# Performance work log

Hardware: AMD Instinct MI355X
Metric: run time of the kernel (lower is better)

The kernel has to match this reference:

```python
import jax, jax.numpy as jnp
import numpy as np

P = 16          # patch size
D = 256         # emb dim
NH = 4          # attention heads
DH = D // NH    # head dim
GS = 4          # LE-fusion group size
EPS = 1e-5
ALPHA = 1.0
DELTA = 1.0
BETA = 1.0


def setup_inputs() -> dict:
    key = jax.random.key(0)
    ks = jax.random.split(key, 12)
    B, C, H, W = 8, 1, 256, 256
    s = 0.02
    return {
        "x": jax.random.normal(ks[0], (B, C, H, W), jnp.float32),
        # patch embed as matmul over flattened patches (equivalent to Conv2d k=s=P)
        "Wp": jax.random.normal(ks[1], (C * P * P, D), jnp.float32) * s,
        "bp": jnp.zeros((D,), jnp.float32),
        "ln_g": jnp.ones((D,), jnp.float32),
        "ln_b": jnp.zeros((D,), jnp.float32),
        "Wq": jax.random.normal(ks[2], (D, D), jnp.float32) * s,
        "bq": jnp.zeros((D,), jnp.float32),
        "Wk": jax.random.normal(ks[3], (D, D), jnp.float32) * s,
        "bk": jnp.zeros((D,), jnp.float32),
        "Wv": jax.random.normal(ks[4], (D, D), jnp.float32) * s,
        "bv": jnp.zeros((D,), jnp.float32),
        "Wo": jax.random.normal(ks[5], (D, D), jnp.float32) * s,
        "bo": jnp.zeros((D,), jnp.float32),
    }


def _forward(x, Wp, bp, ln_g, ln_b, Wq, bq, Wk, bk, Wv, bv, Wo, bo):
    B, C, H, W = x.shape
    nh, nw = H // P, W // P
    N = nh * nw
    # --- patch embed: (B,C,H,W) -> (B,N,C*P*P) @ Wp ---
    patches = x.reshape(B, C, nh, P, nw, P).transpose(0, 2, 4, 1, 3, 5)
    patches = patches.reshape(B, N, C * P * P)
    z = patches @ Wp + bp  # (B, N, D)
    # --- NF-Norm: LayerNorm then NeuroFocal scaling ---
    mu = z.mean(-1, keepdims=True)
    var = ((z - mu) ** 2).mean(-1, keepdims=True)
    zn = (z - mu) * jax.lax.rsqrt(var + EPS) * ln_g + ln_b
    mu2 = zn.mean(-1, keepdims=True)
    var2 = ((zn - mu2) ** 2).mean(-1, keepdims=True)
    nf = jnp.abs(zn - mu2).sum(-1, keepdims=True) / (jnp.sqrt(var2 + EPS) + EPS)
    z = zn * (1.0 + nf)
    # --- AG-NFA attention ---
    def split(t):  # (B,N,D) -> (B,NH,N,DH)
        return t.reshape(B, N, NH, DH).transpose(0, 2, 1, 3)
    Q = split(z @ Wq + bq)
    K = split(z @ Wk + bk)
    V = split(z @ Wv + bv)
    qk = jnp.einsum("bhnd,bhmd->bhnm", Q, K)
    logits = qk / jnp.sqrt(jnp.float32(DH))
    mu_q = Q.mean(-1, keepdims=True)
    var_q = ((Q - mu_q) ** 2).mean(-1, keepdims=True)
    sigma_q = jnp.sqrt(var_q + EPS)
    nf_q = jnp.abs(Q - mu_q).sum(-1, keepdims=True) / (sigma_q + EPS)  # (B,NH,N,1)
    # ||Q_n - K_m||^2 = |Q|^2 + |K|^2 - 2 Q.K  (avoids O(N^2*d) diff tensor)
    q2 = (Q * Q).sum(-1)  # (B,NH,N)
    k2 = (K * K).sum(-1)  # (B,NH,N)
    omega = q2[..., :, None] + k2[..., None, :] - 2.0 * qk
    omega = omega / (jnp.exp(-DELTA * nf_q) + 1.0)
    A = jax.nn.softmax(logits - ALPHA * omega, axis=-1)
    out = jnp.einsum("bhnm,bhmd->bhnd", A, V)
    out = out.transpose(0, 2, 1, 3).reshape(B, N, D)
    Y = out @ Wo + bo
    # --- LE-Fusion ---
    G = N // GS
    Yg = Y.reshape(B, G, GS, D)
    E = jnp.linalg.norm(Yg, axis=-1)  # (B,G,GS)
    lam = jax.nn.softmax(BETA * E, axis=-1)[..., None]
    return (lam * Yg).sum(axis=2)  # (B, G, D)


def reference(x, Wp, bp, ln_g, ln_b, Wq, bq, Wk, bk, Wv, bv, Wo, bo):
    return _forward(x, Wp, bp, ln_g, ln_b, Wq, bq, Wk, bk, Wv, bv, Wo, bo)
```

## Files before the change

### kernel.cpp

```cpp
#include <hip/hip_runtime.h>

#define EPSF 1e-5f
#define KSTR 68
#define PSTR 260

#define FMA4(ACC, ZS, WV) \
    ACC.x = fmaf(ZS, WV.x, ACC.x); ACC.y = fmaf(ZS, WV.y, ACC.y); \
    ACC.z = fmaf(ZS, WV.z, ACC.z); ACC.w = fmaf(ZS, WV.w, ACC.w);

__global__ __launch_bounds__(512, 2) void ka_patch_nf_qkv(
    const float* __restrict__ x,
    const float* __restrict__ Wp, const float* __restrict__ bp,
    const float* __restrict__ ln_g, const float* __restrict__ ln_b,
    const float* __restrict__ Wq, const float* __restrict__ bq,
    const float* __restrict__ Wk, const float* __restrict__ bk,
    const float* __restrict__ Wv, const float* __restrict__ bv,
    float* __restrict__ Qg, float* __restrict__ Kg, float* __restrict__ Vg)
{
    extern __shared__ float sm[];
    float* zr = sm;
    float* ps = sm + 2048;

    const int tid = threadIdx.x;
    const int kq = tid >> 7, tg = (tid >> 6) & 1, ln = tid & 63;
    const int wave = tid >> 6, lane = tid & 63;
    const int tok0 = blockIdx.x * 8;
    const int tg4 = 4 * tg;

    #pragma unroll
    for (int i = 0; i < 4; ++i) {
        int e = tid + 512 * i;
        int t = e >> 8, dd = e & 255;
        int tk = tok0 + t, b = tk >> 8, n = tk & 255;
        int ph = n >> 4, pw = n & 15, p = dd >> 4, q = dd & 15;
        zr[t * 256 + dd] = x[b * 65536 + (ph * 16 + p) * 256 + pw * 16 + q];
    }
    __syncthreads();

    {
        const float* wr = Wp + kq * 16384 + 4 * ln;
        const float* zb = zr + tg4 * 256 + kq * 64;
        float4 a0 = make_float4(0.f,0.f,0.f,0.f), a1 = a0, a2 = a0, a3 = a0;
        #pragma unroll
        for (int kk = 0; kk < 64; kk += 8) {
            float4 w0 = *(const float4*)(wr + (kk + 0) * 256);
            float4 w1 = *(const float4*)(wr + (kk + 1) * 256);
            float4 w2 = *(const float4*)(wr + (kk + 2) * 256);
            float4 w3 = *(const float4*)(wr + (kk + 3) * 256);
            float4 w4 = *(const float4*)(wr + (kk + 4) * 256);
            float4 w5 = *(const float4*)(wr + (kk + 5) * 256);
            float4 w6 = *(const float4*)(wr + (kk + 6) * 256);
            float4 w7 = *(const float4*)(wr + (kk + 7) * 256);
            float4 zA0 = *(const float4*)(zb + 0 * 256 + kk);
            float4 zA1 = *(const float4*)(zb + 0 * 256 + kk + 4);
            float4 zB0 = *(const float4*)(zb + 1 * 256 + kk);
            float4 zB1 = *(const float4*)(zb + 1 * 256 + kk + 4);
            float4 zC0 = *(const float4*)(zb + 2 * 256 + kk);
            float4 zC1 = *(const float4*)(zb + 2 * 256 + kk + 4);
            float4 zD0 = *(const float4*)(zb + 3 * 256 + kk);
            float4 zD1 = *(const float4*)(zb + 3 * 256 + kk + 4);
            FMA4(a0, zA0.x, w0) FMA4(a0, zA0.y, w1) FMA4(a0, zA0.z, w2) FMA4(a0, zA0.w, w3)
            FMA4(a0, zA1.x, w4) FMA4(a0, zA1.y, w5) FMA4(a0, zA1.z, w6) FMA4(a0, zA1.w, w7)
            FMA4(a1, zB0.x, w0) FMA4(a1, zB0.y, w1) FMA4(a1, zB0.z, w2) FMA4(a1, zB0.w, w3)
            FMA4(a1, zB1.x, w4) FMA4(a1, zB1.y, w5) FMA4(a1, zB1.z, w6) FMA4(a1, zB1.w, w7)
            FMA4(a2, zC0.x, w0) FMA4(a2, zC0.y, w1) FMA4(a2, zC0.z, w2) FMA4(a2, zC0.w, w3)
            FMA4(a2, zC1.x, w4) FMA4(a2, zC1.y, w5) FMA4(a2, zC1.z, w6) FMA4(a2, zC1.w, w7)
            FMA4(a3, zD0.x, w0) FMA4(a3, zD0.y, w1) FMA4(a3, zD0.z, w2) FMA4(a3, zD0.w, w3)
            FMA4(a3, zD1.x, w4) FMA4(a3, zD1.y, w5) FMA4(a3, zD1.z, w6) FMA4(a3, zD1.w, w7)
        }
        float* pp = ps + kq * 2048 + tg4 * 256 + 4 * ln;
        *(float4*)(pp + 0 * 256) = a0;
        *(float4*)(pp + 1 * 256) = a1;
        *(float4*)(pp + 2 * 256) = a2;
        *(float4*)(pp + 3 * 256) = a3;
    }
    __syncthreads();
    {
        int e = tid * 4;
        float4 u0 = *(float4*)(ps + e);
        float4 u1 = *(float4*)(ps + 2048 + e);
        float4 u2 = *(float4*)(ps + 4096 + e);
        float4 u3 = *(float4*)(ps + 6144 + e);
        float4 bb = *(const float4*)(bp + (e & 255));
        float4 z;
        z.x = (u0.x + u1.x) + (u2.x + u3.x) + bb.x;
        z.y = (u0.y + u1.y) + (u2.y + u3.y) + bb.y;
        z.z = (u0.z + u1.z) + (u2.z + u3.z) + bb.z;
        z.w = (u0.w + u1.w) + (u2.w + u3.w) + bb.w;
        *(float4*)(zr + e) = z;
    }
    __syncthreads();

    {
        float g[4], bb2[4], v[4];
        #pragma unroll
        for (int c = 0; c < 4; ++c) { g[c] = ln_g[lane + 64 * c]; bb2[c] = ln_b[lane + 64 * c]; }
        float s = 0.f, ss = 0.f;
        #pragma unroll
        for (int c = 0; c < 4; ++c) { v[c] = zr[wave * 256 + lane + 64 * c]; s += v[c]; ss += v[c] * v[c]; }
        #pragma unroll
        for (int o = 32; o; o >>= 1) { s += __shfl_xor(s, o); ss += __shfl_xor(ss, o); }
        float mu  = s * (1.f / 256.f);
        float var = ss * (1.f / 256.f) - mu * mu;
        float rs  = rsqrtf(var + EPSF);
        float zn[4]; float s2 = 0.f, ss2 = 0.f;
        #pragma unroll
        for (int c = 0; c < 4; ++c) {
            zn[c] = (v[c] - mu) * rs * g[c] + bb2[c];
            s2 += zn[c]; ss2 += zn[c] * zn[c];
        }
        #pragma unroll
        for (int o = 32; o; o >>= 1) { s2 += __shfl_xor(s2, o); ss2 += __shfl_xor(ss2, o); }
        float mu2  = s2 * (1.f / 256.f);
        float var2 = ss2 * (1.f / 256.f) - mu2 * mu2;
        float as = 0.f;
        #pragma unroll
        for (int c = 0; c < 4; ++c) as += fabsf(zn[c] - mu2);
        #pragma unroll
        for (int o = 32; o; o >>= 1) as += __shfl_xor(as, o);
        float nf = as / (sqrtf(var2 + EPSF) + EPSF);
        float sc = 1.f + nf;
        #pragma unroll
        for (int c = 0; c < 4; ++c) zr[wave * 256 + lane + 64 * c] = zn[c] * sc;
    }
    __syncthreads();

    {
        const float* qr = Wq + kq * 16384 + 4 * ln;
        const float* kr = Wk + kq * 16384 + 4 * ln;
        const float* vr = Wv + kq * 16384 + 4 * ln;
        const float* zb = zr + tg4 * 256 + kq * 64;
        float4 aq0 = make_float4(0.f,0.f,0.f,0.f), aq1 = aq0, aq2 = aq0, aq3 = aq0;
        float4 ak0 = aq0, ak1 = aq0, ak2 = aq0, ak3 = aq0;
        float4 av0 = aq0, av1 = aq0, av2 = aq0, av3 = aq0;
        #pragma unroll
        for (int kk = 0; kk < 64; kk += 4) {
            float4 qw0 = *(const float4*)(qr + (kk + 0) * 256);
            float4 qw1 = *(const float4*)(qr + (kk + 1) * 256);
            float4 qw2 = *(const float4*)(qr + (kk + 2) * 256);
            float4 qw3 = *(const float4*)(qr + (kk + 3) * 256);
            float4 kw0 = *(const float4*)(kr + (kk + 0) * 256);
            float4 kw1 = *(const float4*)(kr + (kk + 1) * 256);
            float4 kw2 = *(const float4*)(kr + (kk + 2) * 256);
            float4 kw3 = *(const float4*)(kr + (kk + 3) * 256);
            float4 vw0 = *(const float4*)(vr + (kk + 0) * 256);
            float4 vw1 = *(const float4*)(vr + (kk + 1) * 256);
            float4 vw2 = *(const float4*)(vr + (kk + 2) * 256);
            float4 vw3 = *(const float4*)(vr + (kk + 3) * 256);
            float4 zA = *(const float4*)(zb + 0 * 256 + kk);
            float4 zB = *(const float4*)(zb + 1 * 256 + kk);
            float4 zC = *(const float4*)(zb + 2 * 256 + kk);
            float4 zD = *(const float4*)(zb + 3 * 256 + kk);
            FMA4(aq0, zA.x, qw0) FMA4(aq0, zA.y, qw1) FMA4(aq0, zA.z, qw2) FMA4(aq0, zA.w, qw3)
            FMA4(ak0, zA.x, kw0) FMA4(ak0, zA.y, kw1) FMA4(ak0, zA.z, kw2) FMA4(ak0, zA.w, kw3)
            FMA4(av0, zA.x, vw0) FMA4(av0, zA.y, vw1) FMA4(av0, zA.z, vw2) FMA4(av0, zA.w, vw3)
            FMA4(aq1, zB.x, qw0) FMA4(aq1, zB.y, qw1) FMA4(aq1, zB.z, qw2) FMA4(aq1, zB.w, qw3)
            FMA4(ak1, zB.x, kw0) FMA4(ak1, zB.y, kw1) FMA4(ak1, zB.z, kw2) FMA4(ak1, zB.w, kw3)
            FMA4(av1, zB.x, vw0) FMA4(av1, zB.y, vw1) FMA4(av1, zB.z, vw2) FMA4(av1, zB.w, vw3)
            FMA4(aq2, zC.x, qw0) FMA4(aq2, zC.y, qw1) FMA4(aq2, zC.z, qw2) FMA4(aq2, zC.w, qw3)
            FMA4(ak2, zC.x, kw0) FMA4(ak2, zC.y, kw1) FMA4(ak2, zC.z, kw2) FMA4(ak2, zC.w, kw3)
            FMA4(av2, zC.x, vw0) FMA4(av2, zC.y, vw1) FMA4(av2, zC.z, vw2) FMA4(av2, zC.w, vw3)
            FMA4(aq3, zD.x, qw0) FMA4(aq3, zD.y, qw1) FMA4(aq3, zD.z, qw2) FMA4(aq3, zD.w, qw3)
            FMA4(ak3, zD.x, kw0) FMA4(ak3, zD.y, kw1) FMA4(ak3, zD.z, kw2) FMA4(ak3, zD.w, kw3)
            FMA4(av3, zD.x, vw0) FMA4(av3, zD.y, vw1) FMA4(av3, zD.z, vw2) FMA4(av3, zD.w, vw3)
        }
        float* pq = ps + kq * 2048 + tg4 * 256 + 4 * ln;
        *(float4*)(pq + 0 * 256) = aq0;
        *(float4*)(pq + 1 * 256) = aq1;
        *(float4*)(pq + 2 * 256) = aq2;
        *(float4*)(pq + 3 * 256) = aq3;
        float* pk = pq + 8192;
        *(float4*)(pk + 0 * 256) = ak0;
        *(float4*)(pk + 1 * 256) = ak1;
        *(float4*)(pk + 2 * 256) = ak2;
        *(float4*)(pk + 3 * 256) = ak3;
        float* pv = pq + 16384;
        *(float4*)(pv + 0 * 256) = av0;
        *(float4*)(pv + 1 * 256) = av1;
        *(float4*)(pv + 2 * 256) = av2;
        *(float4*)(pv + 3 * 256) = av3;
    }
    __syncthreads();

    {
        int e = tid * 4, t = e >> 8, d0 = e & 255;
        int tk = tok0 + t, b = tk >> 8, n = tk & 255;
        int h = d0 >> 6, dh = d0 & 63;
        #pragma unroll
        for (int mat = 0; mat < 3; ++mat) {
            const float* pr = ps + mat * 8192;
            float4 u0 = *(float4*)(pr + e);
            float4 u1 = *(float4*)(pr + 2048 + e);
            float4 u2 = *(float4*)(pr + 4096 + e);
            float4 u3 = *(float4*)(pr + 6144 + e);
            const float* bsrc = (mat == 0) ? bq : (mat == 1) ? bk : bv;
            float4 bb = *(const float4*)(bsrc + d0);
            float4 o;
            o.x = (u0.x + u1.x) + (u2.x + u3.x) + bb.x;
            o.y = (u0.y + u1.y) + (u2.y + u3.y) + bb.y;
            o.z = (u0.z + u1.z) + (u2.z + u3.z) + bb.z;
            o.w = (u0.w + u1.w) + (u2.w + u3.w) + bb.w;
            float* gout = ((mat == 0) ? Qg : (mat == 1) ? Kg : Vg)
                        + ((b * 4 + h) * 256 + n) * 64 + dh;
            *(float4*)gout = o;
        }
    }
}

__global__ __launch_bounds__(512, 2) void kb_attn(
    const float* __restrict__ Qg, const float* __restrict__ Kg,
    const float* __restrict__ Vg, float* __restrict__ Og)
{
    extern __shared__ float lds[];
    float* Kl = lds;
    float* k2 = lds + 256 * KSTR;
    float* Pl = lds;

    const int tid = threadIdx.x;
    const int xcd = blockIdx.x & 7, slot = blockIdx.x >> 3;
    const int bh = xcd * 4 + (slot >> 3);
    const int qt = slot & 7;

    const float* Qb = Qg + (bh * 256 + qt * 32) * 64;
    const float* Kb = Kg + bh * 16384;
    const float* Vb = Vg + bh * 16384;

    const int q = tid >> 4;
    const int r = tid & 15;

    {
        const float4* Ks = (const float4*)Kb;
        #pragma unroll
        for (int i = 0; i < 8; ++i) {
            int flat = tid + 512 * i;
            int row = flat >> 4, c4 = flat & 15;
            *(float4*)(Kl + row * KSTR + c4 * 4) = Ks[flat];
        }
    }
    __syncthreads();

    {
        int row = tid >> 1, half = tid & 1;
        const float* kp = Kl + row * KSTR + half * 32;
        float ssq = 0.f;
        #pragma unroll
        for (int c = 0; c < 8; ++c) {
            float4 kv = *(const float4*)(kp + 4 * c);
            ssq += kv.x*kv.x + kv.y*kv.y + kv.z*kv.z + kv.w*kv.w;
        }
        ssq += __shfl_xor(ssq, 1);
        if (half == 0) k2[row] = ssq;
    }

    float4 Qr[16];
    {
        const float4* Qp = (const float4*)(Qb + q * 64);
        #pragma unroll
        for (int c = 0; c < 16; ++c) Qr[c] = Qp[c];
    }
    float fq, gq, iq;
    {
        float s = 0.f, ss = 0.f;
        #pragma unroll
        for (int c = 0; c < 16; ++c) {
            float4 v = Qr[c];
            s  += v.x + v.y + v.z + v.w;
            ss += v.x*v.x + v.y*v.y + v.z*v.z + v.w*v.w;
        }
        float mu = s * (1.f / 64.f);
        float as = 0.f;
        #pragma unroll
        for (int c = 0; c < 16; ++c) {
            float4 v = Qr[c];
            as += fabsf(v.x - mu) + fabsf(v.y - mu)
                + fabsf(v.z - mu) + fabsf(v.w - mu);
        }
        float var = ss * (1.f / 64.f) - mu * mu;
        float sg  = sqrtf(var + EPSF);
        float nf  = as / (sg + EPSF);
        float inv = 1.f / (__expf(-nf) + 1.f);
        fq = 0.125f + 2.f * inv;
        gq = ss * inv;
        iq = inv;
    }
    __syncthreads();

    float s_[16];
    #pragma unroll
    for (int j = 0; j < 16; ++j) {
        int m = r + 16 * j;
        const float* kp = Kl + m * KSTR;
        float acc = 0.f;
        #pragma unroll
        for (int c = 0; c < 16; ++c) {
            float4 kv = *(const float4*)(kp + 4 * c);
            acc += Qr[c].x*kv.x + Qr[c].y*kv.y + Qr[c].z*kv.z + Qr[c].w*kv.w;
        }
        s_[j] = acc * fq - gq - k2[m] * iq;
    }

    float M = s_[0];
    #pragma unroll
    for (int j = 1; j < 16; ++j) M = fmaxf(M, s_[j]);
    #pragma unroll
    for (int o = 1; o < 16; o <<= 1) M = fmaxf(M, __shfl_xor(M, o));
    float L = 0.f;
    #pragma unroll
    for (int j = 0; j < 16; ++j) { s_[j] = __expf(s_[j] - M); L += s_[j]; }
    #pragma unroll
    for (int o = 1; o < 16; o <<= 1) L += __shfl_xor(L, o);
    float invL = 1.f / L;

    __syncthreads();
    #pragma unroll
    for (int j = 0; j < 16; ++j) Pl[q * PSTR + r + 16 * j] = s_[j] * invL;
    __syncthreads();

    float4 a0 = make_float4(0.f, 0.f, 0.f, 0.f);
    const float* pq = Pl + q * PSTR;
    #pragma unroll 8
    for (int m = 0; m < 256; ++m) {
        float pw = pq[m];
        float4 v = *(const float4*)(Vb + m * 64 + 4 * r);
        a0.x = fmaf(pw, v.x, a0.x); a0.y = fmaf(pw, v.y, a0.y);
        a0.z = fmaf(pw, v.z, a0.z); a0.w = fmaf(pw, v.w, a0.w);
    }
    {
        int b = bh >> 2, h = bh & 3;
        int n = qt * 32 + q;
        float* op = Og + (b * 256 + n) * 256 + h * 64 + 4 * r;
        *(float4*)op = a0;
    }
}

__global__ __launch_bounds__(512, 2) void kc_wo_le(
    const float* __restrict__ Og, const float* __restrict__ Wo,
    const float* __restrict__ bo, float* __restrict__ out)
{
    __shared__ __align__(16) float sm[2048 + 8192 + 8];
    float* yr  = sm;
    float* ps  = sm + 2048;
    float* red = sm + 10240;

    const int tid = threadIdx.x;
    const int kq = tid >> 7, tg = (tid >> 6) & 1, ln = tid & 63;
    const int wave = tid >> 6, lane = tid & 63;
    const int tok0 = blockIdx.x * 8;
    const int tg4 = 4 * tg;

    *(float4*)(yr + tid * 4) = *(const float4*)(Og + tok0 * 256 + tid * 4);
    __syncthreads();

    {
        const float* wr = Wo + kq * 16384 + 4 * ln;
        const float* zb = yr + tg4 * 256 + kq * 64;
        float4 a0 = make_float4(0.f,0.f,0.f,0.f), a1 = a0, a2 = a0, a3 = a0;
        #pragma unroll
        for (int kk = 0; kk < 64; kk += 8) {
            float4 w0 = *(const float4*)(wr + (kk + 0) * 256);
            float4 w1 = *(const float4*)(wr + (kk + 1) * 256);
            float4 w2 = *(const float4*)(wr + (kk + 2) * 256);
            float4 w3 = *(const float4*)(wr + (kk + 3) * 256);
            float4 w4 = *(const float4*)(wr + (kk + 4) * 256);
            float4 w5 = *(const float4*)(wr + (kk + 5) * 256);
            float4 w6 = *(const float4*)(wr + (kk + 6) * 256);
            float4 w7 = *(const float4*)(wr + (kk + 7) * 256);
            float4 zA0 = *(const float4*)(zb + 0 * 256 + kk);
            float4 zA1 = *(const float4*)(zb + 0 * 256 + kk + 4);
            float4 zB0 = *(const float4*)(zb + 1 * 256 + kk);
            float4 zB1 = *(const float4*)(zb + 1 * 256 + kk + 4);
            float4 zC0 = *(const float4*)(zb + 2 * 256 + kk);
            float4 zC1 = *(const float4*)(zb + 2 * 256 + kk + 4);
            float4 zD0 = *(const float4*)(zb + 3 * 256 + kk);
            float4 zD1 = *(const float4*)(zb + 3 * 256 + kk + 4);
            FMA4(a0, zA0.x, w0) FMA4(a0, zA0.y, w1) FMA4(a0, zA0.z, w2) FMA4(a0, zA0.w, w3)
            FMA4(a0, zA1.x, w4) FMA4(a0, zA1.y, w5) FMA4(a0, zA1.z, w6) FMA4(a0, zA1.w, w7)
            FMA4(a1, zB0.x, w0) FMA4(a1, zB0.y, w1) FMA4(a1, zB0.z, w2) FMA4(a1, zB0.w, w3)
            FMA4(a1, zB1.x, w4) FMA4(a1, zB1.y, w5) FMA4(a1, zB1.z, w6) FMA4(a1, zB1.w, w7)
            FMA4(a2, zC0.x, w0) FMA4(a2, zC0.y, w1) FMA4(a2, zC0.z, w2) FMA4(a2, zC0.w, w3)
            FMA4(a2, zC1.x, w4) FMA4(a2, zC1.y, w5) FMA4(a2, zC1.z, w6) FMA4(a2, zC1.w, w7)
            FMA4(a3, zD0.x, w0) FMA4(a3, zD0.y, w1) FMA4(a3, zD0.z, w2) FMA4(a3, zD0.w, w3)
            FMA4(a3, zD1.x, w4) FMA4(a3, zD1.y, w5) FMA4(a3, zD1.z, w6) FMA4(a3, zD1.w, w7)
        }
        float* pp = ps + kq * 2048 + tg4 * 256 + 4 * ln;
        *(float4*)(pp + 0 * 256) = a0;
        *(float4*)(pp + 1 * 256) = a1;
        *(float4*)(pp + 2 * 256) = a2;
        *(float4*)(pp + 3 * 256) = a3;
    }
    __syncthreads();
    {
        int e = tid * 4;
        float4 u0 = *(float4*)(ps + e);
        float4 u1 = *(float4*)(ps + 2048 + e);
        float4 u2 = *(float4*)(ps + 4096 + e);
        float4 u3 = *(float4*)(ps + 6144 + e);
        float4 bb = *(const float4*)(bo + (e & 255));
        float4 y;
        y.x = (u0.x + u1.x) + (u2.x + u3.x) + bb.x;
        y.y = (u0.y + u1.y) + (u2.y + u3.y) + bb.y;
        y.z = (u0.z + u1.z) + (u2.z + u3.z) + bb.z;
        y.w = (u0.w + u1.w) + (u2.w + u3.w) + bb.w;
        *(float4*)(yr + e) = y;
    }
    __syncthreads();
    {
        float ssq = 0.f;
        #pragma unroll
        for (int c = 0; c < 4; ++c) {
            float v = yr[wave * 256 + lane + 64 * c];
            ssq += v * v;
        }
        #pragma unroll
        for (int o = 32; o; o >>= 1) ssq += __shfl_xor(ssq, o);
        if (lane == 0) red[wave] = sqrtf(ssq);
    }
    __syncthreads();
    {
        int g = tid >> 8, d = tid & 255;
        float e0 = red[4 * g], e1 = red[4 * g + 1], e2 = red[4 * g + 2], e3 = red[4 * g + 3];
        float m = fmaxf(fmaxf(e0, e1), fmaxf(e2, e3));
        float x0 = __expf(e0 - m), x1 = __expf(e1 - m), x2 = __expf(e2 - m), x3 = __expf(e3 - m);
        float inv = 1.f / (x0 + x1 + x2 + x3);
        float val = (x0 * yr[(4 * g) * 256 + d] + x1 * yr[(4 * g + 1) * 256 + d]
                   + x2 * yr[(4 * g + 2) * 256 + d] + x3 * yr[(4 * g + 3) * 256 + d]) * inv;
        out[(blockIdx.x * 2 + g) * 256 + d] = val;
    }
}

extern "C" void kernel_launch(void* const* d_in, const int* in_sizes, int n_in,
                              void* d_out, int out_size, void* d_ws, size_t ws_size,
                              hipStream_t stream) {
    const float* x    = (const float*)d_in[0];
    const float* Wp   = (const float*)d_in[1];
    const float* bp   = (const float*)d_in[2];
    const float* ln_g = (const float*)d_in[3];
    const float* ln_b = (const float*)d_in[4];
    const float* Wq   = (const float*)d_in[5];
    const float* bq   = (const float*)d_in[6];
    const float* Wk   = (const float*)d_in[7];
    const float* bk   = (const float*)d_in[8];
    const float* Wv   = (const float*)d_in[9];
    const float* bv   = (const float*)d_in[10];
    const float* Wo   = (const float*)d_in[11];
    const float* bo   = (const float*)d_in[12];
    float* out = (float*)d_out;

    float* ws = (float*)d_ws;
    const size_t TKD = 2048 * 64 * 4;
    float* Qg = ws;
    float* Kg = ws + TKD;
    float* Vg = ws + 2 * TKD;
    float* Og = ws + 3 * TKD;

    const int ka_lds = (2048 + 3 * 4 * 2048) * 4;
    const int kb_lds = (256 * KSTR + 256) * 4;
    (void)hipFuncSetAttribute((const void*)ka_patch_nf_qkv,
                              hipFuncAttributeMaxDynamicSharedMemorySize, ka_lds);
    (void)hipFuncSetAttribute((const void*)kb_attn,
                              hipFuncAttributeMaxDynamicSharedMemorySize, kb_lds);

    ka_patch_nf_qkv<<<256, 512, ka_lds, stream>>>(x, Wp, bp, ln_g, ln_b,
                                                  Wq, bq, Wk, bk, Wv, bv, Qg, Kg, Vg);
    kb_attn<<<256, 512, kb_lds, stream>>>(Qg, Kg, Vg, Og);
    kc_wo_le<<<256, 512, 0, stream>>>(Og, Wo, bo, out);
}
```

Baseline: 60.70 us.

## Fuse three kernels into one cooperative kernel with grid syncs

Merges the patch/NF/QKV, attention and Wo/LE-fusion kernels into a single cooperative launch of 256 blocks, with grid.sync() between the stages in place of kernel boundaries. The aim is to remove launch overhead and the gaps between the three dependent kernels. In exchange the whole grid must be co-resident, LDS sizing is set to the largest stage, and grid-wide barriers carry their own cost.

```diff
diff --git a/kernel.cpp b/kernel.cpp
--- a/kernel.cpp
+++ b/kernel.cpp
@@ -1,4 +1,7 @@
 #include <hip/hip_runtime.h>
+#include <hip/hip_cooperative_groups.h>
+
+namespace cg = cooperative_groups;
 
 #define EPSF 1e-5f
 #define KSTR 68
@@ -8,423 +11,425 @@
     ACC.x = fmaf(ZS, WV.x, ACC.x); ACC.y = fmaf(ZS, WV.y, ACC.y); \
     ACC.z = fmaf(ZS, WV.z, ACC.z); ACC.w = fmaf(ZS, WV.w, ACC.w);
 
-__global__ __launch_bounds__(512, 2) void ka_patch_nf_qkv(
+__global__ __launch_bounds__(512, 2) void mega(
     const float* __restrict__ x,
     const float* __restrict__ Wp, const float* __restrict__ bp,
     const float* __restrict__ ln_g, const float* __restrict__ ln_b,
     const float* __restrict__ Wq, const float* __restrict__ bq,
     const float* __restrict__ Wk, const float* __restrict__ bk,
     const float* __restrict__ Wv, const float* __restrict__ bv,
-    float* __restrict__ Qg, float* __restrict__ Kg, float* __restrict__ Vg)
+    const float* __restrict__ Wo, const float* __restrict__ bo,
+    float* __restrict__ Qg, float* __restrict__ Kg, float* __restrict__ Vg,
+    float* __restrict__ Og, float* __restrict__ out)
 {
     extern __shared__ float sm[];
-    float* zr = sm;
-    float* ps = sm + 2048;
+    cg::grid_group grid = cg::this_grid();
 
     const int tid = threadIdx.x;
-    const int kq = tid >> 7, tg = (tid >> 6) & 1, ln = tid & 63;
-    const int wave = tid >> 6, lane = tid & 63;
-    const int tok0 = blockIdx.x * 8;
-    const int tg4 = 4 * tg;
-
-    #pragma unroll
-    for (int i = 0; i < 4; ++i) {
-        int e = tid + 512 * i;
-        int t = e >> 8, dd = e & 255;
-        int tk = tok0 + t, b = tk >> 8, n = tk & 255;
-        int ph = n >> 4, pw = n & 15, p = dd >> 4, q = dd & 15;
-        zr[t * 256 + dd] = x[b * 65536 + (ph * 16 + p) * 256 + pw * 16 + q];
+    const int bid = blockIdx.x;
+
+    {
+        float* zr = sm;
+        float* ps = sm + 2048;
+
+        const int kq = tid >> 7, tg = (tid >> 6) & 1, ln = tid & 63;
+        const int wave = tid >> 6, lane = tid & 63;
+        const int tok0 = bid * 8;
+        const int tg4 = 4 * tg;
+
+        #pragma unroll
+        for (int i = 0; i < 4; ++i) {
+            int e = tid + 512 * i;
+            int t = e >> 8, dd = e & 255;
+            int tk = tok0 + t, b = tk >> 8, n = tk & 255;
+            int ph = n >> 4, pw = n & 15, p = dd >> 4, q = dd & 15;
+            zr[t * 256 + dd] = x[b * 65536 + (ph * 16 + p) * 256 + pw * 16 + q];
+        }
+        __syncthreads();
+
+        {
+            const float* wr = Wp + kq * 16384 + 4 * ln;
+            const float* zb = zr + tg4 * 256 + kq * 64;
+            float4 a0 = make_float4(0.f,0.f,0.f,0.f), a1 = a0, a2 = a0, a3 = a0;
+            #pragma unroll
+            for (int kk = 0; kk < 64; kk += 8) {
+                float4 w0 = *(const float4*)(wr + (kk + 0) * 256);
+                float4 w1 = *(const float4*)(wr + (kk + 1) * 256);
+                float4 w2 = *(const float4*)(wr + (kk + 2) * 256);
+                float4 w3 = *(const float4*)(wr + (kk + 3) * 256);
+                float4 w4 = *(const float4*)(wr + (kk + 4) * 256);
+                float4 w5 = *(const float4*)(wr + (kk + 5) * 256);
+                float4 w6 = *(const float4*)(wr + (kk + 6) * 256);
+                float4 w7 = *(const float4*)(wr + (kk + 7) * 256);
+                float4 zA0 = *(const float4*)(zb + 0 * 256 + kk);
+                float4 zA1 = *(const float4*)(zb + 0 * 256 + kk + 4);
+                float4 zB0 = *(const float4*)(zb + 1 * 256 + kk);
+                float4 zB1 = *(const float4*)(zb + 1 * 256 + kk + 4);
+                float4 zC0 = *(const float4*)(zb + 2 * 256 + kk);
+                float4 zC1 = *(const float4*)(zb + 2 * 256 + kk + 4);
+                float4 zD0 = *(const float4*)(zb + 3 * 256 + kk);
+                float4 zD1 = *(const float4*)(zb + 3 * 256 + kk + 4);
+                FMA4(a0, zA0.x, w0) FMA4(a0, zA0.y, w1) FMA4(a0, zA0.z, w2) FMA4(a0, zA0.w, w3)
+                FMA4(a0, zA1.x, w4) FMA4(a0, zA1.y, w5) FMA4(a0, zA1.z, w6) FMA4(a0, zA1.w, w7)
+                FMA4(a1, zB0.x, w0) FMA4(a1, zB0.y, w1) FMA4(a1, zB0.z, w2) FMA4(a1, zB0.w, w3)
+                FMA4(a1, zB1.x, w4) FMA4(a1, zB1.y, w5) FMA4(a1, zB1.z, w6) FMA4(a1, zB1.w, w7)
+                FMA4(a2, zC0.x, w0) FMA4(a2, zC0.y, w1) FMA4(a2, zC0.z, w2) FMA4(a2, zC0.w, w3)
+                FMA4(a2, zC1.x, w4) FMA4(a2, zC1.y, w5) FMA4(a2, zC1.z, w6) FMA4(a2, zC1.w, w7)
+                FMA4(a3, zD0.x, w0) FMA4(a3, zD0.y, w1) FMA4(a3, zD0.z, w2) FMA4(a3, zD0.w, w3)
+                FMA4(a3, zD1.x, w4) FMA4(a3, zD1.y, w5) FMA4(a3, zD1.z, w6) FMA4(a3, zD1.w, w7)
+            }
+            float* pp = ps + kq * 2048 + tg4 * 256 + 4 * ln;
+            *(float4*)(pp + 0 * 256) = a0;
+            *(float4*)(pp + 1 * 256) = a1;
+            *(float4*)(pp + 2 * 256) = a2;
+            *(float4*)(pp + 3 * 256) = a3;
+        }
+        __syncthreads();
+        {
+            int e = tid * 4;
+            float4 u0 = *(float4*)(ps + e);
+            float4 u1 = *(float4*)(ps + 2048 + e);
+            float4 u2 = *(float4*)(ps + 4096 + e);
+            float4 u3 = *(float4*)(ps + 6144 + e);
+            float4 bb = *(const float4*)(bp + (e & 255));
+            float4 z;
+            z.x = (u0.x + u1.x) + (u2.x + u3.x) + bb.x;
+            z.y = (u0.y + u1.y) + (u2.y + u3.y) + bb.y;
+            z.z = (u0.z + u1.z) + (u2.z + u3.z) + bb.z;
+            z.w = (u0.w + u1.w) + (u2.w + u3.w) + bb.w;
+            *(float4*)(zr + e) = z;
+        }
+        __syncthreads();
+
+        {
+            float g[4], bb2[4], v[4];
+            #pragma unroll
+            for (int c = 0; c < 4; ++c) { g[c] = ln_g[lane + 64 * c]; bb2[c] = ln_b[lane + 64 * c]; }
+            float s = 0.f, ss = 0.f;
+            #pragma unroll
+            for (int c = 0; c < 4; ++c) { v[c] = zr[wave * 256 + lane + 64 * c]; s += v[c]; ss += v[c] * v[c]; }
+            #pragma unroll
+            for (int o = 32; o; o >>= 1) { s += __shfl_xor(s, o); ss += __shfl_xor(ss, o); }
+            float mu  = s * (1.f / 256.f);
+            float var = ss * (1.f / 256.f) - mu * mu;
+            float rs  = rsqrtf(var + EPSF);
+            float zn[4]; float s2 = 0.f, ss2 = 0.f;
+            #pragma unroll
+            for (int c = 0; c < 4; ++c) {
+                zn[c] = (v[c] - mu) * rs * g[c] + bb2[c];
+                s2 += zn[c]; ss2 += zn[c] * zn[c];
+            }
+            #pragma unroll
+            for (int o = 32; o; o >>= 1) { s2 += __shfl_xor(s2, o); ss2 += __shfl_xor(ss2, o); }
+            float mu2  = s2 * (1.f / 256.f);
+            float var2 = ss2 * (1.f / 256.f) - mu2 * mu2;
+            float as = 0.f;
+            #pragma unroll
+            for (int c = 0; c < 4; ++c) as += fabsf(zn[c] - mu2);
+            #pragma unroll
+            for (int o = 32; o; o >>= 1) as += __shfl_xor(as, o);
+            float nf = as / (sqrtf(var2 + EPSF) + EPSF);
+            float sc = 1.f + nf;
+            #pragma unroll
+            for (int c = 0; c < 4; ++c) zr[wave * 256 + lane + 64 * c] = zn[c] * sc;
+        }
+        __syncthreads();
+
+        {
+            const float* qr = Wq + kq * 16384 + 4 * ln;
+            const float* kr = Wk + kq * 16384 + 4 * ln;
+            const float* vr = Wv + kq * 16384 + 4 * ln;
+            const float* zb = zr + tg4 * 256 + kq * 64;
+            float4 aq0 = make_float4(0.f,0.f,0.f,0.f), aq1 = aq0, aq2 = aq0, aq3 = aq0;
+            float4 ak0 = aq0, ak1 = aq0, ak2 = aq0, ak3 = aq0;
+            float4 av0 = aq0, av1 = aq0, av2 = aq0, av3 = aq0;
+            #pragma unroll
+            for (int kk = 0; kk < 64; kk += 4) {
+                float4 qw0 = *(const float4*)(qr + (kk + 0) * 256);
+                float4 qw1 = *(const float4*)(qr + (kk + 1) * 256);
+                float4 qw2 = *(const float4*)(qr + (kk + 2) * 256);
+                float4 qw3 = *(const float4*)(qr + (kk + 3) * 256);
+                float4 kw0 = *(const float4*)(kr + (kk + 0) * 256);
+                float4 kw1 = *(const float4*)(kr + (kk + 1) * 256);
+                float4 kw2 = *(const float4*)(kr + (kk + 2) * 256);
+                float4 kw3 = *(const float4*)(kr + (kk + 3) * 256);
+                float4 vw0 = *(const float4*)(vr + (kk + 0) * 256);
+                float4 vw1 = *(const float4*)(vr + (kk + 1) * 256);
+                float4 vw2 = *(const float4*)(vr + (kk + 2) * 256);
+                float4 vw3 = *(const float4*)(vr + (kk + 3) * 256);
+                float4 zA = *(const float4*)(zb + 0 * 256 + kk);
+                float4 zB = *(const float4*)(zb + 1 * 256 + kk);
+                float4 zC = *(const float4*)(zb + 2 * 256 + kk);
+                float4 zD = *(const float4*)(zb + 3 * 256 + kk);
+                FMA4(aq0, zA.x, qw0) FMA4(aq0, zA.y, qw1) FMA4(aq0, zA.z, qw2) FMA4(aq0, zA.w, qw3)
+                FMA4(ak0, zA.x, kw0) FMA4(ak0, zA.y, kw1) FMA4(ak0, zA.z, kw2) FMA4(ak0, zA.w, kw3)
+                FMA4(av0, zA.x, vw0) FMA4(av0, zA.y, vw1) FMA4(av0, zA.z, vw2) FMA4(av0, zA.w, vw3)
+                FMA4(aq1, zB.x, qw0) FMA4(aq1, zB.y, qw1) FMA4(aq1, zB.z, qw2) FMA4(aq1, zB.w, qw3)
+                FMA4(ak1, zB.x, kw0) FMA4(ak1, zB.y, kw1) FMA4(ak1, zB.z, kw2) FMA4(ak1, zB.w, kw3)
+                FMA4(av1, zB.x, vw0) FMA4(av1, zB.y, vw1) FMA4(av1, zB.z, vw2) FMA4(av1, zB.w, vw3)
+                FMA4(aq2, zC.x, qw0) FMA4(aq2, zC.y, qw1) FMA4(aq2, zC.z, qw2) FMA4(aq2, zC.w, qw3)
+                FMA4(ak2, zC.x, kw0) FMA4(ak2, zC.y, kw1) FMA4(ak2, zC.z, kw2) FMA4(ak2, zC.w, kw3)
+                FMA4(av2, zC.x, vw0) FMA4(av2, zC.y, vw1) FMA4(av2, zC.z, vw2) FMA4(av2, zC.w, vw3)
+                FMA4(aq3, zD.x, qw0) FMA4(aq3, zD.y, qw1) FMA4(aq3, zD.z, qw2) FMA4(aq3, zD.w, qw3)
+                FMA4(ak3, zD.x, kw0) FMA4(ak3, zD.y, kw1) FMA4(ak3, zD.z, kw2) FMA4(ak3, zD.w, kw3)
+                FMA4(av3, zD.x, vw0) FMA4(av3, zD.y, vw1) FMA4(av3, zD.z, vw2) FMA4(av3, zD.w, vw3)
+            }
+            float* pq = ps + kq * 2048 + tg4 * 256 + 4 * ln;
+            *(float4*)(pq + 0 * 256) = aq0;
+            *(float4*)(pq + 1 * 256) = aq1;
+            *(float4*)(pq + 2 * 256) = aq2;
+            *(float4*)(pq + 3 * 256) = aq3;
+            float* pk = pq + 8192;
+            *(float4*)(pk + 0 * 256) = ak0;
+            *(float4*)(pk + 1 * 256) = ak1;
+            *(float4*)(pk + 2 * 256) = ak2;
+            *(float4*)(pk + 3 * 256) = ak3;
+            float* pv = pq + 16384;
+            *(float4*)(pv + 0 * 256) = av0;
+            *(float4*)(pv + 1 * 256) = av1;
+            *(float4*)(pv + 2 * 256) = av2;
+            *(float4*)(pv + 3 * 256) = av3;
+        }
+        __syncthreads();
+
+        {
+            int e = tid * 4, t = e >> 8, d0 = e & 255;
+            int tk = tok0 + t, b = tk >> 8, n = tk & 255;
+            int h = d0 >> 6, dh = d0 & 63;
+            #pragma unroll
+            for (int mat = 0; mat < 3; ++mat) {
+                const float* pr = ps + mat * 8192;
+                float4 u0 = *(float4*)(pr + e);
+                float4 u1 = *(float4*)(pr + 2048 + e);
+                float4 u2 = *(float4*)(pr + 4096 + e);
+                float4 u3 = *(float4*)(pr + 6144 + e);
+                const float* bsrc = (mat == 0) ? bq : (mat == 1) ? bk : bv;
+                float4 bb = *(const float4*)(bsrc + d0);
+                float4 o;
+                o.x = (u0.x + u1.x) + (u2.x + u3.x) + bb.x;
+                o.y = (u0.y + u1.y) + (u2.y + u3.y) + bb.y;
+                o.z = (u0.z + u1.z) + (u2.z + u3.z) + bb.z;
+                o.w = (u0.w + u1.w) + (u2.w + u3.w) + bb.w;
+                float* gout = ((mat == 0) ? Qg : (mat == 1) ? Kg : Vg)
+                            + ((b * 4 + h) * 256 + n) * 64 + dh;
+                *(float4*)gout = o;
+            }
+        }
     }
-    __syncthreads();
+
+    grid.sync();
 
     {
-        const float* wr = Wp + kq * 16384 + 4 * ln;
-        const float* zb = zr + tg4 * 256 + kq * 64;
-        float4 a0 = make_float4(0.f,0.f,0.f,0.f), a1 = a0, a2 = a0, a3 = a0;
-        #pragma unroll
-        for (int kk = 0; kk < 64; kk += 8) {
-            float4 w0 = *(const float4*)(wr + (kk + 0) * 256);
-            float4 w1 = *(const float4*)(wr + (kk + 1) * 256);
-            float4 w2 = *(const float4*)(wr + (kk + 2) * 256);
-            float4 w3 = *(const float4*)(wr + (kk + 3) * 256);
-            float4 w4 = *(const float4*)(wr + (kk + 4) * 256);
-            float4 w5 = *(const float4*)(wr + (kk + 5) * 256);
-            float4 w6 = *(const float4*)(wr + (kk + 6) * 256);
-            float4 w7 = *(const float4*)(wr + (kk + 7) * 256);
-            float4 zA0 = *(const float4*)(zb + 0 * 256 + kk);
-            float4 zA1 = *(const float4*)(zb + 0 * 256 + kk + 4);
-            float4 zB0 = *(const float4*)(zb + 1 * 256 + kk);
-            float4 zB1 = *(const float4*)(zb + 1 * 256 + kk + 4);
-            float4 zC0 = *(const float4*)(zb + 2 * 256 + kk);
-            float4 zC1 = *(const float4*)(zb + 2 * 256 + kk + 4);
-            float4 zD0 = *(const float4*)(zb + 3 * 256 + kk);
-            float4 zD1 = *(const float4*)(zb + 3 * 256 + kk + 4);
-            FMA4(a0, zA0.x, w0) FMA4(a0, zA0.y, w1) FMA4(a0, zA0.z, w2) FMA4(a0, zA0.w, w3)
-            FMA4(a0, zA1.x, w4) FMA4(a0, zA1.y, w5) FMA4(a0, zA1.z, w6) FMA4(a0, zA1.w, w7)
-            FMA4(a1, zB0.x, w0) FMA4(a1, zB0.y, w1) FMA4(a1, zB0.z, w2) FMA4(a1, zB0.w, w3)
-            FMA4(a1, zB1.x, w4) FMA4(a1, zB1.y, w5) FMA4(a1, zB1.z, w6) FMA4(a1, zB1.w, w7)
-            FMA4(a2, zC0.x, w0) FMA4(a2, zC0.y, w1) FMA4(a2, zC0.z, w2) FMA4(a2, zC0.w, w3)
-            FMA4(a2, zC1.x, w4) FMA4(a2, zC1.y, w5) FMA4(a2, zC1.z, w6) FMA4(a2, zC1.w, w7)
-            FMA4(a3, zD0.x, w0) FMA4(a3, zD0.y, w1) FMA4(a3, zD0.z, w2) FMA4(a3, zD0.w, w3)
-            FMA4(a3, zD1.x, w4) FMA4(a3, zD1.y, w5) FMA4(a3, zD1.z, w6) FMA4(a3, zD1.w, w7)
-        }
-        float* pp = ps + kq * 2048 + tg4 * 256 + 4 * ln;
-        *(float4*)(pp + 0 * 256) = a0;
-        *(float4*)(pp + 1 * 256) = a1;
-        *(float4*)(pp + 2 * 256) = a2;
-        *(float4*)(pp + 3 * 256) = a3;
+        float* Kl = sm;
+        float* k2 = sm + 256 * KSTR;
+        float* Pl = sm;
+
+        const int xcd = bid & 7, slot = bid >> 3;
+        const int bh = xcd * 4 + (slot >> 3);
+        const int qt = slot & 7;
+
+        const float* Qb = Qg + (bh * 256 + qt * 32) * 64;
+        const float* Kb = Kg + bh * 16384;
+        const float* Vb = Vg + bh * 16384;
+
+        const int q = tid >> 4;
+        const int r = tid & 15;
+
+        {
+            const float4* Ks = (const float4*)Kb;
+            #pragma unroll
+            for (int i = 0; i < 8; ++i) {
+                int flat = tid + 512 * i;
+                int row = flat >> 4, c4 = flat & 15;
+                *(float4*)(Kl + row * KSTR + c4 * 4) = Ks[flat];
+            }
+        }
+        __syncthreads();
+
+        {
+            int row = tid >> 1, half = tid & 1;
+            const float* kp = Kl + row * KSTR + half * 32;
+            float ssq = 0.f;
+            #pragma unroll
+            for (int c = 0; c < 8; ++c) {
+                float4 kv = *(const float4*)(kp + 4 * c);
+                ssq += kv.x*kv.x + kv.y*kv.y + kv.z*kv.z + kv.w*kv.w;
+            }
+            ssq += __shfl_xor(ssq, 1);
+            if (half == 0) k2[row] = ssq;
+        }
+
+        float4 Qr[16];
+        {
+            const float4* Qp = (const float4*)(Qb + q * 64);
+            #pragma unroll
+            for (int c = 0; c < 16; ++c) Qr[c] = Qp[c];
+        }
+        float fq, gq, iq;
+        {
+            float s = 0.f, ss = 0.f;
+            #pragma unroll
+            for (int c = 0; c < 16; ++c) {
+                float4 v = Qr[c];
+                s  += v.x + v.y + v.z + v.w;
+                ss += v.x*v.x + v.y*v.y + v.z*v.z + v.w*v.w;
+            }
+            float mu = s * (1.f / 64.f);
+            float as = 0.f;
+            #pragma unroll
+            for (int c = 0; c < 16; ++c) {
+                float4 v = Qr[c];
+                as += fabsf(v.x - mu) + fabsf(v.y - mu)
+                    + fabsf(v.z - mu) + fabsf(v.w - mu);
+            }
+            float var = ss * (1.f / 64.f) - mu * mu;
+            float sg  = sqrtf(var + EPSF);
+            float nf  = as / (sg + EPSF);
+            float inv = 1.f / (__expf(-nf) + 1.f);
+            fq = 0.125f + 2.f * inv;
+            gq = ss * inv;
+            iq = inv;
+        }
+        __syncthreads();
+
+        float s_[16];
+        #pragma unroll
+        for (int j = 0; j < 16; ++j) {
+            int m = r + 16 * j;
+            const float* kp = Kl + m * KSTR;
+            float acc = 0.f;
+            #pragma unroll
+            for (int c = 0; c < 16; ++c) {
+                float4 kv = *(const float4*)(kp + 4 * c);
+                acc += Qr[c].x*kv.x + Qr[c].y*kv.y + Qr[c].z*kv.z + Qr[c].w*kv.w;
+            }
+            s_[j] = acc * fq - gq - k2[m] * iq;
+        }
+
+        float M = s_[0];
+        #pragma unroll
+        for (int j = 1; j < 16; ++j) M = fmaxf(M, s_[j]);
+        #pragma unroll
+        for (int o = 1; o < 16; o <<= 1) M = fmaxf(M, __shfl_xor(M, o));
+        float L = 0.f;
+        #pragma unroll
+        for (int j = 0; j < 16; ++j) { s_[j] = __expf(s_[j] - M); L += s_[j]; }
+        #pragma unroll
+        for (int o = 1; o < 16; o <<= 1) L += __shfl_xor(L, o);
+        float invL = 1.f / L;
+
+        __syncthreads();
+        #pragma unroll
+        for (int j = 0; j < 16; ++j) Pl[q * PSTR + r + 16 * j] = s_[j] * invL;
+        __syncthreads();
+
+        float4 a0 = make_float4(0.f, 0.f, 0.f, 0.f);
+        const float* pq = Pl + q * PSTR;
+        #pragma unroll 8
+        for (int m = 0; m < 256; ++m) {
+            float pw = pq[m];
+            float4 v = *(const float4*)(Vb + m * 64 + 4 * r);
+            a0.x = fmaf(pw, v.x, a0.x); a0.y = fmaf(pw, v.y, a0.y);
+            a0.z = fmaf(pw, v.z, a0.z); a0.w = fmaf(pw, v.w, a0.w);
+        }
+        {
+            int b = bh >> 2, h = bh & 3;
+            int n = qt * 32 + q;
+            float* op = Og + (b * 256 + n) * 256 + h * 64 + 4 * r;
+            *(float4*)op = a0;
+        }
     }
-    __syncthreads();
+
+    grid.sync();
+
     {
-        int e = tid * 4;
-        float4 u0 = *(float4*)(ps + e);
-        float4 u1 = *(float4*)(ps + 2048 + e);
-        float4 u2 = *(float4*)(ps + 4096 + e);
-        float4 u3 = *(float4*)(ps + 6144 + e);
-        float4 bb = *(const float4*)(bp + (e & 255));
-        float4 z;
-        z.x = (u0.x + u1.x) + (u2.x + u3.x) + bb.x;
-        z.y = (u0.y + u1.y) + (u2.y + u3.y) + bb.y;
-        z.z = (u0.z + u1.z) + (u2.z + u3.z) + bb.z;
-        z.w = (u0.w + u1.w) + (u2.w + u3.w) + bb.w;
-        *(float4*)(zr + e) = z;
-    }
-    __syncthreads();
-
-    {
-        float g[4], bb2[4], v[4];
-        #pragma unroll
-        for (int c = 0; c < 4; ++c) { g[c] = ln_g[lane + 64 * c]; bb2[c] = ln_b[lane + 64 * c]; }
-        float s = 0.f, ss = 0.f;
-        #pragma unroll
-        for (int c = 0; c < 4; ++c) { v[c] = zr[wave * 256 + lane + 64 * c]; s += v[c]; ss += v[c] * v[c]; }
-        #pragma unroll
-        for (int o = 32; o; o >>= 1) { s += __shfl_xor(s, o); ss += __shfl_xor(ss, o); }
-        float mu  = s * (1.f / 256.f);
-        float var = ss * (1.f / 256.f) - mu * mu;
-        float rs  = rsqrtf(var + EPSF);
-        float zn[4]; float s2 = 0.f, ss2 = 0.f;
-        #pragma unroll
-        for (int c = 0; c < 4; ++c) {
-            zn[c] = (v[c] - mu) * rs * g[c] + bb2[c];
-            s2 += zn[c]; ss2 += zn[c] * zn[c];
-        }
-        #pragma unroll
-        for (int o = 32; o; o >>= 1) { s2 += __shfl_xor(s2, o); ss2 += __shfl_xor(ss2, o); }
-        float mu2  = s2 * (1.f / 256.f);
-        float var2 = ss2 * (1.f / 256.f) - mu2 * mu2;
-        float as = 0.f;
-        #pragma unroll
-        for (int c = 0; c < 4; ++c) as += fabsf(zn[c] - mu2);
-        #pragma unroll
-        for (int o = 32; o; o >>= 1) as += __shfl_xor(as, o);
-        float nf = as / (sqrtf(var2 + EPSF) + EPSF);
-        float sc = 1.f + nf;
-        #pragma unroll
-        for (int c = 0; c < 4; ++c) zr[wave * 256 + lane + 64 * c] = zn[c] * sc;
-    }
-    __syncthreads();
-
-    {
-        const float* qr = Wq + kq * 16384 + 4 * ln;
-        const float* kr = Wk + kq * 16384 + 4 * ln;
-        const float* vr = Wv + kq * 16384 + 4 * ln;
-        const float* zb = zr + tg4 * 256 + kq * 64;
-        float4 aq0 = make_float4(0.f,0.f,0.f,0.f), aq1 = aq0, aq2 = aq0, aq3 = aq0;
-        float4 ak0 = aq0, ak1 = aq0, ak2 = aq0, ak3 = aq0;
-        float4 av0 = aq0, av1 = aq0, av2 = aq0, av3 = aq0;
-        #pragma unroll
-        for (int kk = 0; kk < 64; kk += 4) {
-            float4 qw0 = *(const float4*)(qr + (kk + 0) * 256);
-            float4 qw1 = *(const float4*)(qr + (kk + 1) * 256);
-            float4 qw2 = *(const float4*)(qr + (kk + 2) * 256);
-            float4 qw3 = *(const float4*)(qr + (kk + 3) * 256);
-            float4 kw0 = *(const float4*)(kr + (kk + 0) * 256);
-            float4 kw1 = *(const float4*)(kr + (kk + 1) * 256);
-            float4 kw2 = *(const float4*)(kr + (kk + 2) * 256);
-            float4 kw3 = *(const float4*)(kr + (kk + 3) * 256);
-            float4 vw0 = *(const float4*)(vr + (kk + 0) * 256);
-            float4 vw1 = *(const float4*)(vr + (kk + 1) * 256);
-            float4 vw2 = *(const float4*)(vr + (kk + 2) * 256);
-            float4 vw3 = *(const float4*)(vr + (kk + 3) * 256);
-            float4 zA = *(const float4*)(zb + 0 * 256 + kk);
-            float4 zB = *(const float4*)(zb + 1 * 256 + kk);
-            float4 zC = *(const float4*)(zb + 2 * 256 + kk);
-            float4 zD = *(const float4*)(zb + 3 * 256 + kk);
-            FMA4(aq0, zA.x, qw0) FMA4(aq0, zA.y, qw1) FMA4(aq0, zA.z, qw2) FMA4(aq0, zA.w, qw3)
-            FMA4(ak0, zA.x, kw0) FMA4(ak0, zA.y, kw1) FMA4(ak0, zA.z, kw2) FMA4(ak0, zA.w, kw3)
-            FMA4(av0, zA.x, vw0) FMA4(av0, zA.y, vw1) FMA4(av0, zA.z, vw2) FMA4(av0, zA.w, vw3)
-            FMA4(aq1, zB.x, qw0) FMA4(aq1, zB.y, qw1) FMA4(aq1, zB.z, qw2) FMA4(aq1, zB.w, qw3)
-            FMA4(ak1, zB.x, kw0) FMA4(ak1, zB.y, kw1) FMA4(ak1, zB.z, kw2) FMA4(ak1, zB.w, kw3)
-            FMA4(av1, zB.x, vw0) FMA4(av1, zB.y, vw1) FMA4(av1, zB.z, vw2) FMA4(av1, zB.w, vw3)
-            FMA4(aq2, zC.x, qw0) FMA4(aq2, zC.y, qw1) FMA4(aq2, zC.z, qw2) FMA4(aq2, zC.w, qw3)
-            FMA4(ak2, zC.x, kw0) FMA4(ak2, zC.y, kw1) FMA4(ak2, zC.z, kw2) FMA4(ak2, zC.w, kw3)
-            FMA4(av2, zC.x, vw0) FMA4(av2, zC.y, vw1) FMA4(av2, zC.z, vw2) FMA4(av2, zC.w, vw3)
-            FMA4(aq3, zD.x, qw0) FMA4(aq3, zD.y, qw1) FMA4(aq3, zD.z, qw2) FMA4(aq3, zD.w, qw3)
-            FMA4(ak3, zD.x, kw0) FMA4(ak3, zD.y, kw1) FMA4(ak3, zD.z, kw2) FMA4(ak3, zD.w, kw3)
-            FMA4(av3, zD.x, vw0) FMA4(av3, zD.y, vw1) FMA4(av3, zD.z, vw2) FMA4(av3, zD.w, vw3)
-        }
-        float* pq = ps + kq * 2048 + tg4 * 256 + 4 * ln;
-        *(float4*)(pq + 0 * 256) = aq0;
-        *(float4*)(pq + 1 * 256) = aq1;
-        *(float4*)(pq + 2 * 256) = aq2;
-        *(float4*)(pq + 3 * 256) = aq3;
-        float* pk = pq + 8192;
-        *(float4*)(pk + 0 * 256) = ak0;
-        *(float4*)(pk + 1 * 256) = ak1;
-        *(float4*)(pk + 2 * 256) = ak2;
-        *(float4*)(pk + 3 * 256) = ak3;
-        float* pv = pq + 16384;
-        *(float4*)(pv + 0 * 256) = av0;
-        *(float4*)(pv + 1 * 256) = av1;
-        *(float4*)(pv + 2 * 256) = av2;
-        *(float4*)(pv + 3 * 256) = av3;
-    }
-    __syncthreads();
-
-    {
-        int e = tid * 4, t = e >> 8, d0 = e & 255;
-        int tk = tok0 + t, b = tk >> 8, n = tk & 255;
-        int h = d0 >> 6, dh = d0 & 63;
-        #pragma unroll
-        for (int mat = 0; mat < 3; ++mat) {
-            const float* pr = ps + mat * 8192;
-            float4 u0 = *(float4*)(pr + e);
-            float4 u1 = *(float4*)(pr + 2048 + e);
-            float4 u2 = *(float4*)(pr + 4096 + e);
-            float4 u3 = *(float4*)(pr + 6144 + e);
-            const float* bsrc = (mat == 0) ? bq : (mat == 1) ? bk : bv;
-            float4 bb = *(const float4*)(bsrc + d0);
-            float4 o;
-            o.x = (u0.x + u1.x) + (u2.x + u3.x) + bb.x;
-            o.y = (u0.y + u1.y) + (u2.y + u3.y) + bb.y;
-            o.z = (u0.z + u1.z) + (u2.z + u3.z) + bb.z;
-            o.w = (u0.w + u1.w) + (u2.w + u3.w) + bb.w;
-            float* gout = ((mat == 0) ? Qg : (mat == 1) ? Kg : Vg)
-                        + ((b * 4 + h) * 256 + n) * 64 + dh;
-            *(float4*)gout = o;
-        }
-    }
-}
-
-__global__ __launch_bounds__(512, 2) void kb_attn(
-    const float* __restrict__ Qg, const float* __restrict__ Kg,
-    const float* __restrict__ Vg, float* __restrict__ Og)
-{
-    extern __shared__ float lds[];
-    float* Kl = lds;
-    float* k2 = lds + 256 * KSTR;
-    float* Pl = lds;
-
-    const int tid = threadIdx.x;
-    const int xcd = blockIdx.x & 7, slot = blockIdx.x >> 3;
-    const int bh = xcd * 4 + (slot >> 3);
-    const int qt = slot & 7;
-
-    const float* Qb = Qg + (bh * 256 + qt * 32) * 64;
-    const float* Kb = Kg + bh * 16384;
-    const float* Vb = Vg + bh * 16384;
-
-    const int q = tid >> 4;
-    const int r = tid & 15;
-
-    {
-        const float4* Ks = (const float4*)Kb;
-        #pragma unroll
-        for (int i = 0; i < 8; ++i) {
-            int flat = tid + 512 * i;
-            int row = flat >> 4, c4 = flat & 15;
-            *(float4*)(Kl + row * KSTR + c4 * 4) = Ks[flat];
-        }
-    }
-    __syncthreads();
-
-    {
-        int row = tid >> 1, half = tid & 1;
-        const float* kp = Kl + row * KSTR + half * 32;
-        float ssq = 0.f;
-        #pragma unroll
-        for (int c = 0; c < 8; ++c) {
-            float4 kv = *(const float4*)(kp + 4 * c);
-            ssq += kv.x*kv.x + kv.y*kv.y + kv.z*kv.z + kv.w*kv.w;
-        }
-        ssq += __shfl_xor(ssq, 1);
-        if (half == 0) k2[row] = ssq;
-    }
-
-    float4 Qr[16];
-    {
-        const float4* Qp = (const float4*)(Qb + q * 64);
-        #pragma unroll
-        for (int c = 0; c < 16; ++c) Qr[c] = Qp[c];
-    }
-    float fq, gq, iq;
-    {
-        float s = 0.f, ss = 0.f;
-        #pragma unroll
-        for (int c = 0; c < 16; ++c) {
-            float4 v = Qr[c];
-            s  += v.x + v.y + v.z + v.w;
-            ss += v.x*v.x + v.y*v.y + v.z*v.z + v.w*v.w;
-        }
-        float mu = s * (1.f / 64.f);
-        float as = 0.f;
-        #pragma unroll
-        for (int c = 0; c < 16; ++c) {
-            float4 v = Qr[c];
-            as += fabsf(v.x - mu) + fabsf(v.y - mu)
-                + fabsf(v.z - mu) + fabsf(v.w - mu);
-        }
-        float var = ss * (1.f / 64.f) - mu * mu;
-        float sg  = sqrtf(var + EPSF);
-        float nf  = as / (sg + EPSF);
-        float inv = 1.f / (__expf(-nf) + 1.f);
-        fq = 0.125f + 2.f * inv;
-        gq = ss * inv;
-        iq = inv;
-    }
-    __syncthreads();
-
-    float s_[16];
-    #pragma unroll
-    for (int j = 0; j < 16; ++j) {
-        int m = r + 16 * j;
-        const float* kp = Kl + m * KSTR;
-        float acc = 0.f;
-        #pragma unroll
-        for (int c = 0; c < 16; ++c) {
-            float4 kv = *(const float4*)(kp + 4 * c);
-            acc += Qr[c].x*kv.x + Qr[c].y*kv.y + Qr[c].z*kv.z + Qr[c].w*kv.w;
-        }
-        s_[j] = acc * fq - gq - k2[m] * iq;
-    }
-
-    float M = s_[0];
-    #pragma unroll
-    for (int j = 1; j < 16; ++j) M = fmaxf(M, s_[j]);
-    #pragma unroll
-    for (int o = 1; o < 16; o <<= 1) M = fmaxf(M, __shfl_xor(M, o));
-    float L = 0.f;
-    #pragma unroll
-    for (int j = 0; j < 16; ++j) { s_[j] = __expf(s_[j] - M); L += s_[j]; }
-    #pragma unroll
-    for (int o = 1; o < 16; o <<= 1) L += __shfl_xor(L, o);
-    float invL = 1.f / L;
-
-    __syncthreads();
-    #pragma unroll
-    for (int j = 0; j < 16; ++j) Pl[q * PSTR + r + 16 * j] = s_[j] * invL;
-    __syncthreads();
-
-    float4 a0 = make_float4(0.f, 0.f, 0.f, 0.f);
-    const float* pq = Pl + q * PSTR;
-    #pragma unroll 8
-    for (int m = 0; m < 256; ++m) {
-        float pw = pq[m];
-        float4 v = *(const float4*)(Vb + m * 64 + 4 * r);
-        a0.x = fmaf(pw, v.x, a0.x); a0.y = fmaf(pw, v.y, a0.y);
-        a0.z = fmaf(pw, v.z, a0.z); a0.w = fmaf(pw, v.w, a0.w);
-    }
-    {
-        int b = bh >> 2, h = bh & 3;
-        int n = qt * 32 + q;
-        float* op = Og + (b * 256 + n) * 256 + h * 64 + 4 * r;
-        *(float4*)op = a0;
-    }
-}
-
-__global__ __launch_bounds__(512, 2) void kc_wo_le(
-    const float* __restrict__ Og, const float* __restrict__ Wo,
-    const float* __restrict__ bo, float* __restrict__ out)
-{
-    __shared__ __align__(16) float sm[2048 + 8192 + 8];
-    float* yr  = sm;
-    float* ps  = sm + 2048;
-    float* red = sm + 10240;
-
-    const int tid = threadIdx.x;
-    const int kq = tid >> 7, tg = (tid >> 6) & 1, ln = tid & 63;
-    const int wave = tid >> 6, lane = tid & 63;
-    const int tok0 = blockIdx.x * 8;
-    const int tg4 = 4 * tg;
-
-    *(float4*)(yr + tid * 4) = *(const float4*)(Og + tok0 * 256 + tid * 4);
-    __syncthreads();
-
-    {
-        const float* wr = Wo + kq * 16384 + 4 * ln;
-        const float* zb = yr + tg4 * 256 + kq * 64;
-        float4 a0 = make_float4(0.f,0.f,0.f,0.f), a1 = a0, a2 = a0, a3 = a0;
-        #pragma unroll
-        for (int kk = 0; kk < 64; kk += 8) {
-            float4 w0 = *(const float4*)(wr + (kk + 0) * 256);
-            float4 w1 = *(const float4*)(wr + (kk + 1) * 256);
-            float4 w2 = *(const float4*)(wr + (kk + 2) * 256);
-            float4 w3 = *(const float4*)(wr + (kk + 3) * 256);
-            float4 w4 = *(const float4*)(wr + (kk + 4) * 256);
-            float4 w5 = *(const float4*)(wr + (kk + 5) * 256);
-            float4 w6 = *(const float4*)(wr + (kk + 6) * 256);
-            float4 w7 = *(const float4*)(wr + (kk + 7) * 256);
-            float4 zA0 = *(const float4*)(zb + 0 * 256 + kk);
-            float4 zA1 = *(const float4*)(zb + 0 * 256 + kk + 4);
-            float4 zB0 = *(const float4*)(zb + 1 * 256 + kk);
-            float4 zB1 = *(const float4*)(zb + 1 * 256 + kk + 4);
-            float4 zC0 = *(const float4*)(zb + 2 * 256 + kk);
-            float4 zC1 = *(const float4*)(zb + 2 * 256 + kk + 4);
-            float4 zD0 = *(const float4*)(zb + 3 * 256 + kk);
-            float4 zD1 = *(const float4*)(zb + 3 * 256 + kk + 4);
-            FMA4(a0, zA0.x, w0) FMA4(a0, zA0.y, w1) FMA4(a0, zA0.z, w2) FMA4(a0, zA0.w, w3)
-            FMA4(a0, zA1.x, w4) FMA4(a0, zA1.y, w5) FMA4(a0, zA1.z, w6) FMA4(a0, zA1.w, w7)
-            FMA4(a1, zB0.x, w0) FMA4(a1, zB0.y, w1) FMA4(a1, zB0.z, w2) FMA4(a1, zB0.w, w3)
-            FMA4(a1, zB1.x, w4) FMA4(a1, zB1.y, w5) FMA4(a1, zB1.z, w6) FMA4(a1, zB1.w, w7)
-            FMA4(a2, zC0.x, w0) FMA4(a2, zC0.y, w1) FMA4(a2, zC0.z, w2) FMA4(a2, zC0.w, w3)
-            FMA4(a2, zC1.x, w4) FMA4(a2, zC1.y, w5) FMA4(a2, zC1.z, w6) FMA4(a2, zC1.w, w7)
-            FMA4(a3, zD0.x, w0) FMA4(a3, zD0.y, w1) FMA4(a3, zD0.z, w2) FMA4(a3, zD0.w, w3)
-            FMA4(a3, zD1.x, w4) FMA4(a3, zD1.y, w5) FMA4(a3, zD1.z, w6) FMA4(a3, zD1.w, w7)
-        }
-        float* pp = ps + kq * 2048 + tg4 * 256 + 4 * ln;
-        *(float4*)(pp + 0 * 256) = a0;
-        *(float4*)(pp + 1 * 256) = a1;
-        *(float4*)(pp + 2 * 256) = a2;
-        *(float4*)(pp + 3 * 256) = a3;
-    }
-    __syncthreads();
-    {
-        int e = tid * 4;
-        float4 u0 = *(float4*)(ps + e);
-        float4 u1 = *(float4*)(ps + 2048 + e);
-        float4 u2 = *(float4*)(ps + 4096 + e);
-        float4 u3 = *(float4*)(ps + 6144 + e);
-        float4 bb = *(const float4*)(bo + (e & 255));
-        float4 y;
-        y.x = (u0.x + u1.x) + (u2.x + u3.x) + bb.x;
-        y.y = (u0.y + u1.y) + (u2.y + u3.y) + bb.y;
-        y.z = (u0.z + u1.z) + (u2.z + u3.z) + bb.z;
-        y.w = (u0.w + u1.w) + (u2.w + u3.w) + bb.w;
-        *(float4*)(yr + e) = y;
-    }
-    __syncthreads();
-    {
-        float ssq = 0.f;
-        #pragma unroll
-        for (int c = 0; c < 4; ++c) {
-            float v = yr[wave * 256 + lane + 64 * c];
-            ssq += v * v;
-        }
-        #pragma unroll
-        for (int o = 32; o; o >>= 1) ssq += __shfl_xor(ssq, o);
-        if (lane == 0) red[wave] = sqrtf(ssq);
-    }
-    __syncthreads();
-    {
-        int g = tid >> 8, d = tid & 255;
-        float e0 = red[4 * g], e1 = red[4 * g + 1], e2 = red[4 * g + 2], e3 = red[4 * g + 3];
-        float m = fmaxf(fmaxf(e0, e1), fmaxf(e2, e3));
-        float x0 = __expf(e0 - m), x1 = __expf(e1 - m), x2 = __expf(e2 - m), x3 = __expf(e3 - m);
-        float inv = 1.f / (x0 + x1 + x2 + x3);
-        float val = (x0 * yr[(4 * g) * 256 + d] + x1 * yr[(4 * g + 1) * 256 + d]
-                   + x2 * yr[(4 * g + 2) * 256 + d] + x3 * yr[(4 * g + 3) * 256 + d]) * inv;
-        out[(blockIdx.x * 2 + g) * 256 + d] = val;
+        float* yr  = sm;
+        float* ps  = sm + 2048;
+        float* red = sm + 10240;
+
+        const int kq = tid >> 7, tg = (tid >> 6) & 1, ln = tid & 63;
+        const int wave = tid >> 6, lane = tid & 63;
+        const int tok0 = bid * 8;
+        const int tg4 = 4 * tg;
+
+        *(float4*)(yr + tid * 4) = *(const float4*)(Og + tok0 * 256 + tid * 4);
+        __syncthreads();
+
+        {
+            const float* wr = Wo + kq * 16384 + 4 * ln;
+            const float* zb = yr + tg4 * 256 + kq * 64;
+            float4 a0 = make_float4(0.f,0.f,0.f,0.f), a1 = a0, a2 = a0, a3 = a0;
+            #pragma unroll
+            for (int kk = 0; kk < 64; kk += 8) {
+                float4 w0 = *(const float4*)(wr + (kk + 0) * 256);
+                float4 w1 = *(const float4*)(wr + (kk + 1) * 256);
+                float4 w2 = *(const float4*)(wr + (kk + 2) * 256);
+                float4 w3 = *(const float4*)(wr + (kk + 3) * 256);
+                float4 w4 = *(const float4*)(wr + (kk + 4) * 256);
+                float4 w5 = *(const float4*)(wr + (kk + 5) * 256);
+                float4 w6 = *(const float4*)(wr + (kk + 6) * 256);
+                float4 w7 = *(const float4*)(wr + (kk + 7) * 256);
+                float4 zA0 = *(const float4*)(zb + 0 * 256 + kk);
+                float4 zA1 = *(const float4*)(zb + 0 * 256 + kk + 4);
+                float4 zB0 = *(const float4*)(zb + 1 * 256 + kk);
+                float4 zB1 = *(const float4*)(zb + 1 * 256 + kk + 4);
+                float4 zC0 = *(const float4*)(zb + 2 * 256 + kk);
+                float4 zC1 = *(const float4*)(zb + 2 * 256 + kk + 4);
+                float4 zD0 = *(const float4*)(zb + 3 * 256 + kk);
+                float4 zD1 = *(const float4*)(zb + 3 * 256 + kk + 4);
+                FMA4(a0, zA0.x, w0) FMA4(a0, zA0.y, w1) FMA4(a0, zA0.z, w2) FMA4(a0, zA0.w, w3)
+                FMA4(a0, zA1.x, w4) FMA4(a0, zA1.y, w5) FMA4(a0, zA1.z, w6) FMA4(a0, zA1.w, w7)
+                FMA4(a1, zB0.x, w0) FMA4(a1, zB0.y, w1) FMA4(a1, zB0.z, w2) FMA4(a1, zB0.w, w3)
+                FMA4(a1, zB1.x, w4) FMA4(a1, zB1.y, w5) FMA4(a1, zB1.z, w6) FMA4(a1, zB1.w, w7)
+                FMA4(a2, zC0.x, w0) FMA4(a2, zC0.y, w1) FMA4(a2, zC0.z, w2) FMA4(a2, zC0.w, w3)
+                FMA4(a2, zC1.x, w4) FMA4(a2, zC1.y, w5) FMA4(a2, zC1.z, w6) FMA4(a2, zC1.w, w7)
+                FMA4(a3, zD0.x, w0) FMA4(a3, zD0.y, w1) FMA4(a3, zD0.z, w2) FMA4(a3, zD0.w, w3)
+                FMA4(a3, zD1.x, w4) FMA4(a3, zD1.y, w5) FMA4(a3, zD1.z, w6) FMA4(a3, zD1.w, w7)
+            }
+            float* pp = ps + kq * 2048 + tg4 * 256 + 4 * ln;
+            *(float4*)(pp + 0 * 256) = a0;
+            *(float4*)(pp + 1 * 256) = a1;
+            *(float4*)(pp + 2 * 256) = a2;
+            *(float4*)(pp + 3 * 256) = a3;
+        }
+        __syncthreads();
+        {
+            int e = tid * 4;
+            float4 u0 = *(float4*)(ps + e);
+            float4 u1 = *(float4*)(ps + 2048 + e);
+            float4 u2 = *(float4*)(ps + 4096 + e);
+            float4 u3 = *(float4*)(ps + 6144 + e);
+            float4 bb = *(const float4*)(bo + (e & 255));
+            float4 y;
+            y.x = (u0.x + u1.x) + (u2.x + u3.x) + bb.x;
+            y.y = (u0.y + u1.y) + (u2.y + u3.y) + bb.y;
+            y.z = (u0.z + u1.z) + (u2.z + u3.z) + bb.z;
+            y.w = (u0.w + u1.w) + (u2.w + u3.w) + bb.w;
+            *(float4*)(yr + e) = y;
+        }
+        __syncthreads();
+        {
+            float ssq = 0.f;
+            #pragma unroll
+            for (int c = 0; c < 4; ++c) {
+                float v = yr[wave * 256 + lane + 64 * c];
+                ssq += v * v;
+            }
+            #pragma unroll
+            for (int o = 32; o; o >>= 1) ssq += __shfl_xor(ssq, o);
+            if (lane == 0) red[wave] = sqrtf(ssq);
+        }
+        __syncthreads();
+        {
+            int g = tid >> 8, d = tid & 255;
+            float e0 = red[4 * g], e1 = red[4 * g + 1], e2 = red[4 * g + 2], e3 = red[4 * g + 3];
+            float m = fmaxf(fmaxf(e0, e1), fmaxf(e2, e3));
+            float x0 = __expf(e0 - m), x1 = __expf(e1 - m), x2 = __expf(e2 - m), x3 = __expf(e3 - m);
+            float inv = 1.f / (x0 + x1 + x2 + x3);
+            float val = (x0 * yr[(4 * g) * 256 + d] + x1 * yr[(4 * g + 1) * 256 + d]
+                       + x2 * yr[(4 * g + 2) * 256 + d] + x3 * yr[(4 * g + 3) * 256 + d]) * inv;
+            out[(bid * 2 + g) * 256 + d] = val;
+        }
     }
 }
 
@@ -447,21 +452,21 @@
     float* out = (float*)d_out;
 
     float* ws = (float*)d_ws;
-    const size_t TKD = 2048 * 64 * 4;
     float* Qg = ws;
-    float* Kg = ws + TKD;
-    float* Vg = ws + 2 * TKD;
-    float* Og = ws + 3 * TKD;
-
-    const int ka_lds = (2048 + 3 * 4 * 2048) * 4;
-    const int kb_lds = (256 * KSTR + 256) * 4;
-    (void)hipFuncSetAttribute((const void*)ka_patch_nf_qkv,
-                              hipFuncAttributeMaxDynamicSharedMemorySize, ka_lds);
-    (void)hipFuncSetAttribute((const void*)kb_attn,
-                              hipFuncAttributeMaxDynamicSharedMemorySize, kb_lds);
-
-    ka_patch_nf_qkv<<<256, 512, ka_lds, stream>>>(x, Wp, bp, ln_g, ln_b,
-                                                  Wq, bq, Wk, bk, Wv, bv, Qg, Kg, Vg);
-    kb_attn<<<256, 512, kb_lds, stream>>>(Qg, Kg, Vg, Og);
-    kc_wo_le<<<256, 512, 0, stream>>>(Og, Wo, bo, out);
+    float* Kg = ws + 524288;
+    float* Vg = ws + 524288 * 2;
+    float* Og = ws + 524288 * 3;
+
+    const int lds_bytes = (2048 + 3 * 4 * 2048) * 4;
+    (void)hipFuncSetAttribute((const void*)mega,
+                              hipFuncAttributeMaxDynamicSharedMemorySize, lds_bytes);
+
+    void* args[] = {
+        (void*)&x, (void*)&Wp, (void*)&bp, (void*)&ln_g, (void*)&ln_b,
+        (void*)&Wq, (void*)&bq, (void*)&Wk, (void*)&bk, (void*)&Wv, (void*)&bv,
+        (void*)&Wo, (void*)&bo,
+        (void*)&Qg, (void*)&Kg, (void*)&Vg, (void*)&Og, (void*)&out
+    };
+    (void)hipLaunchCooperativeKernel((const void*)mega, dim3(256), dim3(512),
+                                     args, lds_bytes, stream);
 }
```

After: 132.4 us. +118.1%, slower.
